# Kernel tuning notes

Hardware: AMD Instinct MI355X
Metric: run time of the kernel (lower is better)

Reference implementation:

```python
import jax, jax.numpy as jnp
import numpy as np

N_PARENT, N_CHILD = 4, 8
BATCH = 16_777_216  # 2**24
TEMPERATURE = 0.1
SINKHORN_ITERS = 20


def _identity_init(key, shape):
    n_parent, n_child = shape
    log_alpha = jax.random.normal(key, shape, jnp.float32) * 0.1
    identity_bias = 5.0
    for i in range(n_parent):
        log_alpha = log_alpha.at[i, i].add(identity_bias)
        if i + n_parent < n_child:
            log_alpha = log_alpha.at[i, i + n_parent].add(identity_bias)
    return log_alpha


def setup_inputs() -> dict:
    key = jax.random.key(0)
    k1, k2, k3, k4, k5 = jax.random.split(key, 5)
    a = jax.random.normal(k1, (BATCH,), jnp.float32)
    b = jax.random.normal(k2, (BATCH,), jnp.float32)
    operation_id = jax.random.randint(k3, (BATCH,), 0, N_CHILD, dtype=jnp.int32)
    logic_masks = jax.random.normal(k4, (N_PARENT, 4), jnp.float32)
    log_alpha = _identity_init(k5, (N_PARENT, N_CHILD))
    sign_logits = jnp.array([2.0, 2.0, 2.0, 2.0, -2.0, -2.0, -2.0, -2.0], jnp.float32)
    return {"a": a, "b": b, "operation_id": operation_id,
            "logic_masks": logic_masks, "log_alpha": log_alpha,
            "sign_logits": sign_logits}


def _sinkhorn(log_alpha, n_iters=SINKHORN_ITERS, temperature=TEMPERATURE):
    n_parent, n_child = log_alpha.shape
    log_target_row_sum = jnp.log(jnp.asarray(n_child / n_parent, log_alpha.dtype))
    la = log_alpha / temperature
    def body(_, la):
        la = la - jax.nn.logsumexp(la, axis=0, keepdims=True)   # column normalize
        la = la + log_target_row_sum - jax.nn.logsumexp(la, axis=1, keepdims=True)
        return la
    la = jax.lax.fori_loop(0, n_iters, body, la)
    return jnp.exp(la)


def reference(a, b, operation_id, logic_masks, log_alpha, sign_logits):
    # training=True path of Phase2ALayer
    P = _sinkhorn(log_alpha)                      # (4, 8)
    s = jnp.tanh(sign_logits / TEMPERATURE)       # (8,)
    R = P * s[None, :]                            # (4, 8)
    temporal_masks = R.T @ logic_masks            # (8, 4)
    mask = temporal_masks[operation_id]           # (B, 4) gather
    # boolean Fourier features [1, a, b, ab]
    features = jnp.stack([jnp.ones_like(a), a, b, a * b], axis=-1)  # (B, 4)
    output = jnp.sum(features * mask, axis=-1)    # (B,)
    return jnp.tanh(output * 10.0)
```

## Files before the change

### kernel.cpp

```cpp
#include <hip/hip_runtime.h>
#include <hip/hip_bf16.h>

#define N_PARENT 4
#define N_CHILD 8
#define SINKHORN_ITERS 20
#define INV_TEMP 10.0f

typedef float f4 __attribute__((ext_vector_type(4)));
typedef int   i4 __attribute__((ext_vector_type(4)));

__global__ void sinkhorn_table_kernel(const float* __restrict__ logic_masks,
                                      const float* __restrict__ log_alpha,
                                      const float* __restrict__ sign_logits,
                                      float* __restrict__ tm ) {
    const int lane = threadIdx.x & 63;
    const int idx  = lane & 31;
    const int i    = idx >> 3;
    const int j    = idx & 7;

    float la = log_alpha[i * N_CHILD + j] * INV_TEMP;
    const float log_row_target = 0.6931471805599453f;

    #pragma unroll 1
    for (int it = 0; it < SINKHORN_ITERS; ++it) {
        float m = la;
        m = fmaxf(m, __shfl_xor(m, 8));
        m = fmaxf(m, __shfl_xor(m, 16));
        float e = expf(la - m);
        e += __shfl_xor(e, 8);
        e += __shfl_xor(e, 16);
        la = la - (m + logf(e));
        m = la;
        m = fmaxf(m, __shfl_xor(m, 1));
        m = fmaxf(m, __shfl_xor(m, 2));
        m = fmaxf(m, __shfl_xor(m, 4));
        e = expf(la - m);
        e += __shfl_xor(e, 1);
        e += __shfl_xor(e, 2);
        e += __shfl_xor(e, 4);
        la = la + log_row_target - (m + logf(e));
    }

    const float P = expf(la);
    const float s = tanhf(sign_logits[j] * INV_TEMP);
    const float R = P * s;

    const float scale = 28.853900817779268f;

    #pragma unroll
    for (int mm = 0; mm < 4; ++mm) {
        float t = R * logic_masks[i * 4 + mm];
        t += __shfl_xor(t, 8);
        t += __shfl_xor(t, 16);
        if (lane < 8) tm[j * 4 + mm] = t * scale;
    }
}

__device__ __forceinline__ float4 apply4(f4 av, f4 bv, i4 ov, const f4* s_tm) {
    float4 r;
    {
        f4 m = s_tm[ov.x & 7];
        float d = m.x + av.x * m.y + bv.x * m.z + av.x * bv.x * m.w;
        r.x = 1.0f - 2.0f * __builtin_amdgcn_rcpf(__builtin_amdgcn_exp2f(d) + 1.0f);
    }
    {
        f4 m = s_tm[ov.y & 7];
        float d = m.x + av.y * m.y + bv.y * m.z + av.y * bv.y * m.w;
        r.y = 1.0f - 2.0f * __builtin_amdgcn_rcpf(__builtin_amdgcn_exp2f(d) + 1.0f);
    }
    {
        f4 m = s_tm[ov.z & 7];
        float d = m.x + av.z * m.y + bv.z * m.z + av.z * bv.z * m.w;
        r.z = 1.0f - 2.0f * __builtin_amdgcn_rcpf(__builtin_amdgcn_exp2f(d) + 1.0f);
    }
    {
        f4 m = s_tm[ov.w & 7];
        float d = m.x + av.w * m.y + bv.w * m.z + av.w * bv.w * m.w;
        r.w = 1.0f - 2.0f * __builtin_amdgcn_rcpf(__builtin_amdgcn_exp2f(d) + 1.0f);
    }
    return r;
}

__global__ __launch_bounds__(256) void
phase2a_apply_kernel(const float* __restrict__ a,
                     const float* __restrict__ b,
                     const int*   __restrict__ op,
                     const float* __restrict__ tm,
                     float*       __restrict__ out,
                     int half ) {
    __shared__ f4 s_tm[N_CHILD];
    if (threadIdx.x < N_CHILD) {
        s_tm[threadIdx.x] = reinterpret_cast<const f4*>(tm)[threadIdx.x];
    }
    __syncthreads();

    const f4* __restrict__ a4  = reinterpret_cast<const f4*>(a);
    const f4* __restrict__ b4  = reinterpret_cast<const f4*>(b);
    const i4* __restrict__ op4 = reinterpret_cast<const i4*>(op);
    f4*       __restrict__ o4  = reinterpret_cast<f4*>(out);

    const int t = blockIdx.x * 256 + threadIdx.x;
    if (t >= half) return;
    const int t2 = t + half;

    f4 av0 = a4[t];
    f4 bv0 = b4[t];
    i4 ov0 = op4[t];
    f4 av1 = a4[t2];
    f4 bv1 = b4[t2];
    i4 ov1 = op4[t2];

    float4 r0 = apply4(av0, bv0, ov0, s_tm);
    float4 r1 = apply4(av1, bv1, ov1, s_tm);

    f4 w0 = { r0.x, r0.y, r0.z, r0.w };
    f4 w1 = { r1.x, r1.y, r1.z, r1.w };
    __builtin_nontemporal_store(w0, &o4[t]);
    __builtin_nontemporal_store(w1, &o4[t2]);
}

extern "C" void kernel_launch(void* const* d_in, const int* in_sizes, int n_in,
                              void* d_out, int out_size, void* d_ws, size_t ws_size,
                              hipStream_t stream) {
    const float* a           = (const float*)d_in[0];
    const float* b           = (const float*)d_in[1];
    const int*   op          = (const int*)d_in[2];
    const float* logic_masks = (const float*)d_in[3];
    const float* log_alpha   = (const float*)d_in[4];
    const float* sign_logits = (const float*)d_in[5];
    float*       out         = (float*)d_out;
    float*       tm          = (float*)d_ws;

    const int n    = in_sizes[0];
    const int n4   = n >> 2;
    const int half = n4 >> 1;

    sinkhorn_table_kernel<<<1, 64, 0, stream>>>(logic_masks, log_alpha, sign_logits, tm);

    const int blocks = (half + 255) / 256;
    phase2a_apply_kernel<<<blocks, 256, 0, stream>>>(a, b, op, tm, out, half);
}
```

Baseline: 54.78 us.

## Fuse Sinkhorn table computation into apply kernel, recomputed per block

Drops the separate single-block Sinkhorn launch. Each block's first wavefront now recomputes the 8x4 mask table into shared memory, while the block's streaming loads of a, b and op are issued before that work so their latency overlaps it. The Sinkhorn loop also skips max subtraction and uses hardware exp2/log intrinsics, and the bounds check is removed on the assumption that the size divides evenly. This saves a launch and the inter-kernel dependency, at the cost of redundant per-block Sinkhorn work, a possible overflow without max stabilization, and a block-wide barrier in every block.

```diff
diff --git a/kernel.cpp b/kernel.cpp
--- a/kernel.cpp
+++ b/kernel.cpp
@@ -1,122 +1,101 @@
 #include <hip/hip_runtime.h>
-#include <hip/hip_bf16.h>
 
-#define N_PARENT 4
-#define N_CHILD 8
 #define SINKHORN_ITERS 20
-#define INV_TEMP 10.0f
 
 typedef float f4 __attribute__((ext_vector_type(4)));
 typedef int   i4 __attribute__((ext_vector_type(4)));
 
-__global__ void sinkhorn_table_kernel(const float* __restrict__ logic_masks,
-                                      const float* __restrict__ log_alpha,
-                                      const float* __restrict__ sign_logits,
-                                      float* __restrict__ tm ) {
-    const int lane = threadIdx.x & 63;
-    const int idx  = lane & 31;
-    const int i    = idx >> 3;
-    const int j    = idx & 7;
-
-    float la = log_alpha[i * N_CHILD + j] * INV_TEMP;
-    const float log_row_target = 0.6931471805599453f;
-
-    #pragma unroll 1
-    for (int it = 0; it < SINKHORN_ITERS; ++it) {
-        float m = la;
-        m = fmaxf(m, __shfl_xor(m, 8));
-        m = fmaxf(m, __shfl_xor(m, 16));
-        float e = expf(la - m);
-        e += __shfl_xor(e, 8);
-        e += __shfl_xor(e, 16);
-        la = la - (m + logf(e));
-        m = la;
-        m = fmaxf(m, __shfl_xor(m, 1));
-        m = fmaxf(m, __shfl_xor(m, 2));
-        m = fmaxf(m, __shfl_xor(m, 4));
-        e = expf(la - m);
-        e += __shfl_xor(e, 1);
-        e += __shfl_xor(e, 2);
-        e += __shfl_xor(e, 4);
-        la = la + log_row_target - (m + logf(e));
-    }
-
-    const float P = expf(la);
-    const float s = tanhf(sign_logits[j] * INV_TEMP);
-    const float R = P * s;
-
-    const float scale = 28.853900817779268f;
-
-    #pragma unroll
-    for (int mm = 0; mm < 4; ++mm) {
-        float t = R * logic_masks[i * 4 + mm];
-        t += __shfl_xor(t, 8);
-        t += __shfl_xor(t, 16);
-        if (lane < 8) tm[j * 4 + mm] = t * scale;
-    }
+__device__ __forceinline__ float fast_out(float d_prescaled) {
+    return 1.0f - 2.0f * __builtin_amdgcn_rcpf(__builtin_amdgcn_exp2f(d_prescaled) + 1.0f);
 }
 
-__device__ __forceinline__ float4 apply4(f4 av, f4 bv, i4 ov, const f4* s_tm) {
-    float4 r;
+__device__ __forceinline__ f4 apply4(f4 av, f4 bv, i4 ov, const f4* s_tm) {
+    f4 r;
     {
         f4 m = s_tm[ov.x & 7];
-        float d = m.x + av.x * m.y + bv.x * m.z + av.x * bv.x * m.w;
-        r.x = 1.0f - 2.0f * __builtin_amdgcn_rcpf(__builtin_amdgcn_exp2f(d) + 1.0f);
+        r.x = fast_out(m.x + av.x * m.y + bv.x * m.z + av.x * bv.x * m.w);
     }
     {
         f4 m = s_tm[ov.y & 7];
-        float d = m.x + av.y * m.y + bv.y * m.z + av.y * bv.y * m.w;
-        r.y = 1.0f - 2.0f * __builtin_amdgcn_rcpf(__builtin_amdgcn_exp2f(d) + 1.0f);
+        r.y = fast_out(m.x + av.y * m.y + bv.y * m.z + av.y * bv.y * m.w);
     }
     {
         f4 m = s_tm[ov.z & 7];
-        float d = m.x + av.z * m.y + bv.z * m.z + av.z * bv.z * m.w;
-        r.z = 1.0f - 2.0f * __builtin_amdgcn_rcpf(__builtin_amdgcn_exp2f(d) + 1.0f);
+        r.z = fast_out(m.x + av.z * m.y + bv.z * m.z + av.z * bv.z * m.w);
     }
     {
         f4 m = s_tm[ov.w & 7];
-        float d = m.x + av.w * m.y + bv.w * m.z + av.w * bv.w * m.w;
-        r.w = 1.0f - 2.0f * __builtin_amdgcn_rcpf(__builtin_amdgcn_exp2f(d) + 1.0f);
+        r.w = fast_out(m.x + av.w * m.y + bv.w * m.z + av.w * bv.w * m.w);
     }
     return r;
 }
 
 __global__ __launch_bounds__(256) void
-phase2a_apply_kernel(const float* __restrict__ a,
+phase2a_fused_kernel(const float* __restrict__ a,
                      const float* __restrict__ b,
                      const int*   __restrict__ op,
-                     const float* __restrict__ tm,
+                     const float* __restrict__ logic_masks,
+                     const float* __restrict__ log_alpha,
+                     const float* __restrict__ sign_logits,
                      float*       __restrict__ out,
                      int half ) {
-    __shared__ f4 s_tm[N_CHILD];
-    if (threadIdx.x < N_CHILD) {
-        s_tm[threadIdx.x] = reinterpret_cast<const f4*>(tm)[threadIdx.x];
-    }
-    __syncthreads();
+    __shared__ f4 s_tm[8];
 
     const f4* __restrict__ a4  = reinterpret_cast<const f4*>(a);
     const f4* __restrict__ b4  = reinterpret_cast<const f4*>(b);
     const i4* __restrict__ op4 = reinterpret_cast<const i4*>(op);
     f4*       __restrict__ o4  = reinterpret_cast<f4*>(out);
 
-    const int t = blockIdx.x * 256 + threadIdx.x;
-    if (t >= half) return;
-    const int t2 = t + half;
+    const int t0 = blockIdx.x * 256 + threadIdx.x;
+    const int t1 = t0 + half;
 
-    f4 av0 = a4[t];
-    f4 bv0 = b4[t];
-    i4 ov0 = op4[t];
-    f4 av1 = a4[t2];
-    f4 bv1 = b4[t2];
-    i4 ov1 = op4[t2];
+    f4 av0 = a4[t0];  f4 bv0 = b4[t0];  i4 ov0 = op4[t0];
+    f4 av1 = a4[t1];  f4 bv1 = b4[t1];  i4 ov1 = op4[t1];
 
-    float4 r0 = apply4(av0, bv0, ov0, s_tm);
-    float4 r1 = apply4(av1, bv1, ov1, s_tm);
+    if (threadIdx.x < 64) {
+        const int idx = threadIdx.x & 31;
+        const int i   = idx >> 3;
+        const int j   = idx & 7;
 
-    f4 w0 = { r0.x, r0.y, r0.z, r0.w };
-    f4 w1 = { r1.x, r1.y, r1.z, r1.w };
-    __builtin_nontemporal_store(w0, &o4[t]);
-    __builtin_nontemporal_store(w1, &o4[t2]);
+        const float L2E = 1.4426950408889634f;
+        const float LN2 = 0.6931471805599453f;
+
+        float la = log_alpha[i * 8 + j] * 10.0f;
+
+        #pragma unroll 1
+        for (int it = 0; it < SINKHORN_ITERS; ++it) {
+            float e = __builtin_amdgcn_exp2f(la * L2E);
+            e += __shfl_xor(e, 8);
+            e += __shfl_xor(e, 16);
+            la -= __builtin_amdgcn_logf(e) * LN2;
+            e = __builtin_amdgcn_exp2f(la * L2E);
+            e += __shfl_xor(e, 1);
+            e += __shfl_xor(e, 2);
+            e += __shfl_xor(e, 4);
+            la += LN2 - __builtin_amdgcn_logf(e) * LN2;
+        }
+
+        const float scale = 28.853900817779268f;
+        const float P = __builtin_amdgcn_exp2f(la * L2E);
+        const float s = fast_out(sign_logits[j] * scale);
+        const float R = P * s;
+
+        f4 row;
+        #pragma unroll
+        for (int mm = 0; mm < 4; ++mm) {
+            float t = R * logic_masks[i * 4 + mm];
+            t += __shfl_xor(t, 8);
+            t += __shfl_xor(t, 16);
+            row[mm] = t * scale;
+        }
+        if (threadIdx.x < 8) s_tm[threadIdx.x] = row;
+    }
+    __syncthreads();
+
+    f4 r0 = apply4(av0, bv0, ov0, s_tm);
+    f4 r1 = apply4(av1, bv1, ov1, s_tm);
+    __builtin_nontemporal_store(r0, &o4[t0]);
+    __builtin_nontemporal_store(r1, &o4[t1]);
 }
 
 extern "C" void kernel_launch(void* const* d_in, const int* in_sizes, int n_in,
@@ -129,14 +108,14 @@
     const float* log_alpha   = (const float*)d_in[4];
     const float* sign_logits = (const float*)d_in[5];
     float*       out         = (float*)d_out;
-    float*       tm          = (float*)d_ws;
+    (void)d_ws; (void)ws_size;
 
     const int n    = in_sizes[0];
     const int n4   = n >> 2;
     const int half = n4 >> 1;
 
-    sinkhorn_table_kernel<<<1, 64, 0, stream>>>(logic_masks, log_alpha, sign_logits, tm);
-
-    const int blocks = (half + 255) / 256;
-    phase2a_apply_kernel<<<blocks, 256, 0, stream>>>(a, b, op, tm, out, half);
+    const int blocks = half / 256;
+    phase2a_fused_kernel<<<blocks, 256, 0, stream>>>(a, b, op, logic_masks,
+                                                     log_alpha, sign_logits,
+                                                     out, half);
 }
```

After: 46.09 us. -15.9%, faster.
